# Kernel optimization log

Hardware: AMD Instinct MI355X
Metric: run time of the kernel (lower is better)

## Reference

```python
import jax, jax.numpy as jnp
import numpy as np

CAPS = 16          # num_capsules
DIM = 16           # capsule_dim
NUM_ROUTING = 3
L2_EPS = 1e-12     # tf.nn.l2_normalize epsilon


def setup_inputs() -> dict:
    key = jax.random.key(0)
    k1, k2 = jax.random.split(key)
    inputs = jax.random.normal(k1, (16, 64, 64, 128), dtype=jnp.float32)
    # Conv2D kernel, HWIO layout, fan-in scaled like glorot-ish init
    kernel = jax.random.normal(k2, (3, 3, 128, CAPS * DIM), dtype=jnp.float32) * 0.03
    bias = jnp.zeros((CAPS * DIM,), dtype=jnp.float32)
    return {"inputs": inputs, "kernel": kernel, "bias": bias}


def reference(inputs, kernel, bias):
    # Conv2D(caps*dim, 3x3, padding='same', activation='relu'), channels_last
    x = jax.lax.conv_general_dilated(
        inputs, kernel, window_strides=(1, 1), padding="SAME",
        dimension_numbers=("NHWC", "HWIO", "NHWC"))
    x = jax.nn.relu(x + bias)
    B, H, W, _ = x.shape
    x = x.reshape(B, H * W, CAPS, DIM)            # (B, N, C, D)
    b = jnp.zeros((B, H * W, CAPS), dtype=x.dtype)
    v = None
    for _ in range(NUM_ROUTING):
        c = jax.nn.softmax(b, axis=-1)             # over capsules
        s = jnp.einsum("bnc,bncd->bcd", c, x)      # weighted sum over spatial
        # tf.nn.l2_normalize along last axis
        v = s * jax.lax.rsqrt(jnp.maximum(jnp.sum(s * s, axis=-1, keepdims=True), L2_EPS))
        b = b + jnp.einsum("bncd,bcd->bnc", x, v)  # agreement update
    # tile v over spatial dims: (B,1,1,C*D) -> (B,H,W,C*D)
    out = jnp.broadcast_to(v.reshape(B, 1, 1, CAPS * DIM), (B, H, W, CAPS * DIM))
    return out
```

## Files before the change

kernel.cpp:

```cpp
#include <hip/hip_runtime.h>
#include <hip/hip_bf16.h>

typedef unsigned short u16;
typedef unsigned int   u32;

typedef __bf16 bf16x8 __attribute__((ext_vector_type(8)));
typedef float  f32x4  __attribute__((ext_vector_type(4)));

__device__ __forceinline__ u16 f2b(float f) {
    __hip_bfloat16 h = __float2bfloat16(f);
    u16 u; __builtin_memcpy(&u, &h, 2); return u;
}
__device__ __forceinline__ float blo(u32 u) { return __uint_as_float(u << 16); }
__device__ __forceinline__ float bhi(u32 u) { return __uint_as_float(u & 0xffff0000u); }

__global__ void k_prep(const float* __restrict__ wk,
                       u16* __restrict__ BF, float* __restrict__ stats) {
    int bx = blockIdx.x, tid = threadIdx.x;
    if (bx < 1152) {
        int t = bx * 256 + tid;
        int j  = t & 7;
        int n  = (t >> 3) & 255;
        int q  = (t >> 11) & 3;
        int kk = (t >> 13) & 3;
        int p  = t >> 15;
        BF[t] = f2b(wk[(p * 128 + kk * 32 + q * 8 + j) * 256 + n]);
    } else {
        stats[(bx - 1152) * 256 + tid] = 0.f;
    }
}

__launch_bounds__(256, 3)
__global__ void k_conv(const float* __restrict__ in, const u16* __restrict__ BF,
                       const float* __restrict__ bias,
                       u16* __restrict__ X, float* __restrict__ s0) {
    __shared__ u16 ldsA[12672];
    const int t = threadIdx.x;
    const int lane = t & 63, wid = t >> 6;
    const int q = lane >> 4, l15 = lane & 15;
    const int bb = blockIdx.x >> 6;
    const int h  = blockIdx.x & 63;
    const int wn0 = wid << 6;

#define STAGE(S) { \
    const int sb0 = wid * 396; \
    _Pragma("unroll") for (int i = 0; i < 7; ++i) { \
        int slot = sb0 + i * 64 + lane; \
        if (i < 6 || lane < 12) { \
            int pr = slot / 528; int rem = slot - pr * 528; \
            int wp = rem >> 3, cs = rem & 7; \
            int gc = (S) * 8 + (cs ^ (wp & 7)); \
            int y = h + pr - 1, x = wp - 1; \
            int inb = ((unsigned)y < 64u) & ((unsigned)x < 64u); \
            int ys = inb ? y : 0, xs = inb ? x : 0; \
            const float4* s4 = (const float4*)(in + \
                (((bb * 64 + ys) * 64 + xs) * 128 + gc * 8)); \
            float4 f0 = s4[0], f1 = s4[1]; \
            float zf = inb ? 1.f : 0.f; \
            u16 ov[8]; \
            ov[0]=f2b(f0.x*zf); ov[1]=f2b(f0.y*zf); ov[2]=f2b(f0.z*zf); ov[3]=f2b(f0.w*zf); \
            ov[4]=f2b(f1.x*zf); ov[5]=f2b(f1.y*zf); ov[6]=f2b(f1.z*zf); ov[7]=f2b(f1.w*zf); \
            uint4 wv; __builtin_memcpy(&wv, ov, 16); \
            *(uint4*)((char*)ldsA + slot * 16) = wv; \
        } \
    } }

#define LOADB4(B, P, S, KK) { \
    _Pragma("unroll") for (int ni = 0; ni < 4; ++ni) \
        B[ni] = *(const bf16x8*)(BFl + (P) * 32768 + \
                                 ((S) * 2 + (KK)) * 8192 + ni * 128); }

#define COMP4(B, DH, DW, KK) { \
    bf16x8 af[4]; \
    _Pragma("unroll") for (int mi = 0; mi < 4; ++mi) { \
        int wp = mi * 16 + l15 + (DW); \
        int swz = ((KK) * 4 + q) ^ (wp & 7); \
        af[mi] = *(const bf16x8*)((const char*)ldsA + \
            (((DH) * 528 + wp * 8 + swz) << 4)); \
    } \
    _Pragma("unroll") for (int mi = 0; mi < 4; ++mi) \
    _Pragma("unroll") for (int ni = 0; ni < 4; ++ni) \
        acc[mi][ni] = __builtin_amdgcn_mfma_f32_16x16x32_bf16( \
            af[mi], B[ni], acc[mi][ni], 0, 0, 0); }

#define HALF(S) { \
    LOADB4(B0, 0, S, 0); \
    LOADB4(B1, 0, S, 1); COMP4(B0, 0, 0, 0); \
    LOADB4(B0, 1, S, 0); COMP4(B1, 0, 0, 1); \
    LOADB4(B1, 1, S, 1); COMP4(B0, 0, 1, 0); \
    LOADB4(B0, 2, S, 0); COMP4(B1, 0, 1, 1); \
    LOADB4(B1, 2, S, 1); COMP4(B0, 0, 2, 0); \
    LOADB4(B0, 3, S, 0); COMP4(B1, 0, 2, 1); \
    LOADB4(B1, 3, S, 1); COMP4(B0, 1, 0, 0); \
    LOADB4(B0, 4, S, 0); COMP4(B1, 1, 0, 1); \
    LOADB4(B1, 4, S, 1); COMP4(B0, 1, 1, 0); \
    LOADB4(B0, 5, S, 0); COMP4(B1, 1, 1, 1); \
    LOADB4(B1, 5, S, 1); COMP4(B0, 1, 2, 0); \
    LOADB4(B0, 6, S, 0); COMP4(B1, 1, 2, 1); \
    LOADB4(B1, 6, S, 1); COMP4(B0, 2, 0, 0); \
    LOADB4(B0, 7, S, 0); COMP4(B1, 2, 0, 1); \
    LOADB4(B1, 7, S, 1); COMP4(B0, 2, 1, 0); \
    LOADB4(B0, 8, S, 0); COMP4(B1, 2, 1, 1); \
    LOADB4(B1, 8, S, 1); COMP4(B0, 2, 2, 0); \
                         COMP4(B1, 2, 2, 1); }

    const u16* BFl = BF + (q * 2048 + (wn0 + l15) * 8);

    f32x4 zero = {0.f, 0.f, 0.f, 0.f};
    f32x4 acc[4][4];
    #pragma unroll
    for (int mi = 0; mi < 4; ++mi)
        #pragma unroll
        for (int ni = 0; ni < 4; ++ni) acc[mi][ni] = zero;

    bf16x8 B0[4], B1[4];

    STAGE(0);
    __syncthreads();
    HALF(0);
    __syncthreads();

    STAGE(1);
    __syncthreads();
    HALF(1);

    float bv[4];
    #pragma unroll
    for (int ni = 0; ni < 4; ++ni) bv[ni] = bias[wn0 + ni * 16 + l15];
    float colsum[4] = {0.f, 0.f, 0.f, 0.f};
    u16* xrow = X + (((bb << 12) + (h << 6) + q * 4) * 256) + wn0 + l15;
    #pragma unroll
    for (int mi = 0; mi < 4; ++mi) {
        #pragma unroll
        for (int rr = 0; rr < 4; ++rr) {
            u16* xp = xrow + (mi * 16 + rr) * 256;
            #pragma unroll
            for (int ni = 0; ni < 4; ++ni) {
                float v = acc[mi][ni][rr] + bv[ni];
                v = v > 0.f ? v : 0.f;
                xp[ni * 16] = f2b(v);
                colsum[ni] += v;
            }
        }
    }
    #pragma unroll
    for (int ni = 0; ni < 4; ++ni) {
        float c = colsum[ni];
        c += __shfl_xor(c, 16);
        c += __shfl_xor(c, 32);
        if (lane < 16) atomicAdd(&s0[bb * 256 + wn0 + ni * 16 + l15], c);
    }
#undef STAGE
#undef LOADB4
#undef COMP4
#undef HALF
}

__launch_bounds__(256, 4)
__global__ void k_pass(const u16* __restrict__ X, const float* __restrict__ Sa,
                       const float* __restrict__ Sb, float* __restrict__ Sout,
                       int use2) {
    __shared__ float vs[272];
    __shared__ float red[4 * 272];
    const int t = threadIdx.x, b = blockIdx.y, chunk = blockIdx.x;
    const int c = t & 15, nl = t >> 4;
    const int lane = t & 63, wid = t >> 6;
    {
        float sa = Sa[b * 256 + t];
        float ss = sa * sa;
        #pragma unroll
        for (int off = 1; off < 16; off <<= 1) ss += __shfl_xor(ss, off);
        ss = ss < 1e-12f ? 1e-12f : ss;
        float vv = sa / sqrtf(ss);
        if (use2) {
            float sb = Sb[b * 256 + t];
            float s2v = sb * sb;
            #pragma unroll
            for (int off = 1; off < 16; off <<= 1) s2v += __shfl_xor(s2v, off);
            s2v = s2v < 1e-12f ? 1e-12f : s2v;
            vv += sb / sqrtf(s2v);
        }
        vs[(t >> 4) * 17 + (t & 15)] = vv;
    }
    const u16* xbase = X + ((b << 12) + chunk * 64 + nl) * 256 + c * 16;
    uint4 pa[8];
    #pragma unroll
    for (int r = 0; r < 4; ++r) {
        pa[2 * r]     = ((const uint4*)(xbase + r * 4096))[0];
        pa[2 * r + 1] = ((const uint4*)(xbase + r * 4096))[1];
    }
    __syncthreads();
    float vr[16];
    #pragma unroll
    for (int d = 0; d < 16; ++d) vr[d] = vs[c * 17 + d];

    float acc[16];
    #pragma unroll
    for (int d = 0; d < 16; ++d) acc[d] = 0.f;

    #pragma unroll
    for (int r = 0; r < 4; ++r) {
        u32 us[8];
        __builtin_memcpy(us, &pa[2 * r], 32);
        float xf[16];
        #pragma unroll
        for (int j = 0; j < 8; ++j) { xf[2*j] = blo(us[j]); xf[2*j+1] = bhi(us[j]); }
        float bvv = 0.f;
        #pragma unroll
        for (int d = 0; d < 16; ++d) bvv += xf[d] * vr[d];
        float e = __expf(bvv);
        float sm = e;
        #pragma unroll
        for (int off = 1; off < 16; off <<= 1) sm += __shfl_xor(sm, off);
        float w = e / sm;
        #pragma unroll
        for (int d = 0; d < 16; ++d) acc[d] += w * xf[d];
    }
    #pragma unroll
    for (int d = 0; d < 16; ++d) {
        acc[d] += __shfl_xor(acc[d], 16);
        acc[d] += __shfl_xor(acc[d], 32);
    }
    if (lane < 16) {
        #pragma unroll
        for (int d = 0; d < 16; ++d) red[wid * 272 + lane * 17 + d] = acc[d];
    }
    __syncthreads();
    {
        int c2 = t >> 4, d2 = t & 15;
        float tot = red[c2 * 17 + d2]       + red[272 + c2 * 17 + d2]
                  + red[544 + c2 * 17 + d2] + red[816 + c2 * 17 + d2];
        atomicAdd(&Sout[b * 256 + t], tot);
    }
}

__launch_bounds__(256, 4)
__global__ void k_bcast(const float* __restrict__ S, float* __restrict__ Out) {
    __shared__ float vls[256];
    int t = threadIdx.x, bx = blockIdx.x, b = blockIdx.y;
    float s = S[b * 256 + t];
    float ss = s * s;
    #pragma unroll
    for (int off = 1; off < 16; off <<= 1) ss += __shfl_xor(ss, off);
    ss = ss < 1e-12f ? 1e-12f : ss;
    vls[t] = s / sqrtf(ss);
    __syncthreads();
    float4 myv = ((const float4*)vls)[t & 63];
    float4* o = (float4*)Out + (long)b * 262144 + bx * 4096;
    #pragma unroll
    for (int j = 0; j < 16; ++j) o[j * 256 + t] = myv;
}

extern "C" void kernel_launch(void* const* d_in, const int* in_sizes, int n_in,
                              void* d_out, int out_size, void* d_ws, size_t ws_size,
                              hipStream_t stream) {
    const float* in   = (const float*)d_in[0];
    const float* wk   = (const float*)d_in[1];
    const float* bias = (const float*)d_in[2];
    float* out = (float*)d_out;
    char* ws = (char*)d_ws;

    const size_t OFF_BF  = 0;
    const size_t OFF_X   = 589824;
    const size_t OFF_ST  = 34144256;
    const size_t NEEDED  = OFF_ST + 3 * 16384;
    if (ws_size < NEEDED) return;

    u16* BF  = (u16*)(ws + OFF_BF);
    u16* X   = (u16*)(ws + OFF_X);
    float* s0 = (float*)(ws + OFF_ST);
    float* s2 = s0 + 4096;
    float* s3 = s2 + 4096;

    k_prep <<<1200, 256, 0, stream>>>(wk, BF, s0);
    k_conv <<<1024, 256, 0, stream>>>(in, BF, bias, X, s0);
    k_pass <<<dim3(64, 16), 256, 0, stream>>>(X, s0, s0, s2, 0);
    k_pass <<<dim3(64, 16), 256, 0, stream>>>(X, s0, s2, s3, 1);
    k_bcast<<<dim3(64, 16), 256, 0, stream>>>(s3, out);
}
```

Baseline: 181.9 us.

## Stage full input channel slab once with 512-thread blocks split over rows

The conv kernel now uses 512 threads (8 waves arranged 2x4) per output row. Each wave computes 32 pixels by 64 channels instead of 64 by 64. All 128 input channels are staged into LDS in a single pass, with every global load issued before the conversion and stores. This removes the second staging phase and two barriers and halves the accumulator registers per wave. The cost is twice the LDS per block and twice the B-fragment traffic per output, since each weight fragment now feeds only two M-tiles.

```diff
diff --git a/kernel.cpp b/kernel.cpp
--- a/kernel.cpp
+++ b/kernel.cpp
@@ -30,107 +30,129 @@
     }
 }
 
-__launch_bounds__(256, 3)
+__launch_bounds__(512, 4)
 __global__ void k_conv(const float* __restrict__ in, const u16* __restrict__ BF,
                        const float* __restrict__ bias,
                        u16* __restrict__ X, float* __restrict__ s0) {
-    __shared__ u16 ldsA[12672];
+    __shared__ u16 ldsA[25344];
     const int t = threadIdx.x;
     const int lane = t & 63, wid = t >> 6;
     const int q = lane >> 4, l15 = lane & 15;
+    const int wr = wid >> 2;
+    const int wc = wid & 3;
     const int bb = blockIdx.x >> 6;
     const int h  = blockIdx.x & 63;
-    const int wn0 = wid << 6;
-
-#define STAGE(S) { \
-    const int sb0 = wid * 396; \
+    const int wn0 = wc << 6;
+
+#define STAGE_ALL() { \
+    float4 fa[7], fb[7]; float zf[7]; \
     _Pragma("unroll") for (int i = 0; i < 7; ++i) { \
-        int slot = sb0 + i * 64 + lane; \
-        if (i < 6 || lane < 12) { \
-            int pr = slot / 528; int rem = slot - pr * 528; \
-            int wp = rem >> 3, cs = rem & 7; \
-            int gc = (S) * 8 + (cs ^ (wp & 7)); \
-            int y = h + pr - 1, x = wp - 1; \
-            int inb = ((unsigned)y < 64u) & ((unsigned)x < 64u); \
-            int ys = inb ? y : 0, xs = inb ? x : 0; \
-            const float4* s4 = (const float4*)(in + \
-                (((bb * 64 + ys) * 64 + xs) * 128 + gc * 8)); \
-            float4 f0 = s4[0], f1 = s4[1]; \
-            float zf = inb ? 1.f : 0.f; \
+        int slot = i * 512 + t; \
+        int ok = (i < 6) | (t < 96); \
+        int pr = slot / 1056; int rem = slot - pr * 1056; \
+        int wp = rem >> 4, cs = rem & 15; \
+        int gc = cs ^ (wp & 7); \
+        int y = h + pr - 1, x = wp - 1; \
+        int inb = ok & ((((unsigned)y < 64u) & ((unsigned)x < 64u)) ? 1 : 0); \
+        int ys = inb ? y : 0, xs = inb ? x : 0; \
+        const float4* s4 = (const float4*)(in + \
+            (((bb * 64 + ys) * 64 + xs) * 128 + gc * 8)); \
+        fa[i] = s4[0]; fb[i] = s4[1]; \
+        zf[i] = inb ? 1.f : 0.f; \
+    } \
+    _Pragma("unroll") for (int i = 0; i < 7; ++i) { \
+        if (i < 6 || t < 96) { \
+            int slot = i * 512 + t; \
             u16 ov[8]; \
-            ov[0]=f2b(f0.x*zf); ov[1]=f2b(f0.y*zf); ov[2]=f2b(f0.z*zf); ov[3]=f2b(f0.w*zf); \
-            ov[4]=f2b(f1.x*zf); ov[5]=f2b(f1.y*zf); ov[6]=f2b(f1.z*zf); ov[7]=f2b(f1.w*zf); \
+            ov[0]=f2b(fa[i].x*zf[i]); ov[1]=f2b(fa[i].y*zf[i]); \
+            ov[2]=f2b(fa[i].z*zf[i]); ov[3]=f2b(fa[i].w*zf[i]); \
+            ov[4]=f2b(fb[i].x*zf[i]); ov[5]=f2b(fb[i].y*zf[i]); \
+            ov[6]=f2b(fb[i].z*zf[i]); ov[7]=f2b(fb[i].w*zf[i]); \
             uint4 wv; __builtin_memcpy(&wv, ov, 16); \
             *(uint4*)((char*)ldsA + slot * 16) = wv; \
         } \
     } }
 
-#define LOADB4(B, P, S, KK) { \
+#define LOADB4(B, P, G) { \
     _Pragma("unroll") for (int ni = 0; ni < 4; ++ni) \
-        B[ni] = *(const bf16x8*)(BFl + (P) * 32768 + \
-                                 ((S) * 2 + (KK)) * 8192 + ni * 128); }
-
-#define COMP4(B, DH, DW, KK) { \
-    bf16x8 af[4]; \
-    _Pragma("unroll") for (int mi = 0; mi < 4; ++mi) { \
-        int wp = mi * 16 + l15 + (DW); \
-        int swz = ((KK) * 4 + q) ^ (wp & 7); \
+        B[ni] = *(const bf16x8*)(BFl + (P) * 32768 + (G) * 8192 + ni * 128); }
+
+#define COMP4(B, DH, DW, G) { \
+    bf16x8 af[2]; \
+    _Pragma("unroll") for (int mi = 0; mi < 2; ++mi) { \
+        int wp = wr * 32 + mi * 16 + l15 + (DW); \
+        int swz = ((G) * 4 + q) ^ (wp & 7); \
         af[mi] = *(const bf16x8*)((const char*)ldsA + \
-            (((DH) * 528 + wp * 8 + swz) << 4)); \
+            (((DH) * 1056 + wp * 16 + swz) << 4)); \
     } \
-    _Pragma("unroll") for (int mi = 0; mi < 4; ++mi) \
+    _Pragma("unroll") for (int mi = 0; mi < 2; ++mi) \
     _Pragma("unroll") for (int ni = 0; ni < 4; ++ni) \
         acc[mi][ni] = __builtin_amdgcn_mfma_f32_16x16x32_bf16( \
             af[mi], B[ni], acc[mi][ni], 0, 0, 0); }
 
-#define HALF(S) { \
-    LOADB4(B0, 0, S, 0); \
-    LOADB4(B1, 0, S, 1); COMP4(B0, 0, 0, 0); \
-    LOADB4(B0, 1, S, 0); COMP4(B1, 0, 0, 1); \
-    LOADB4(B1, 1, S, 1); COMP4(B0, 0, 1, 0); \
-    LOADB4(B0, 2, S, 0); COMP4(B1, 0, 1, 1); \
-    LOADB4(B1, 2, S, 1); COMP4(B0, 0, 2, 0); \
-    LOADB4(B0, 3, S, 0); COMP4(B1, 0, 2, 1); \
-    LOADB4(B1, 3, S, 1); COMP4(B0, 1, 0, 0); \
-    LOADB4(B0, 4, S, 0); COMP4(B1, 1, 0, 1); \
-    LOADB4(B1, 4, S, 1); COMP4(B0, 1, 1, 0); \
-    LOADB4(B0, 5, S, 0); COMP4(B1, 1, 1, 1); \
-    LOADB4(B1, 5, S, 1); COMP4(B0, 1, 2, 0); \
-    LOADB4(B0, 6, S, 0); COMP4(B1, 1, 2, 1); \
-    LOADB4(B1, 6, S, 1); COMP4(B0, 2, 0, 0); \
-    LOADB4(B0, 7, S, 0); COMP4(B1, 2, 0, 1); \
-    LOADB4(B1, 7, S, 1); COMP4(B0, 2, 1, 0); \
-    LOADB4(B0, 8, S, 0); COMP4(B1, 2, 1, 1); \
-    LOADB4(B1, 8, S, 1); COMP4(B0, 2, 2, 0); \
-                         COMP4(B1, 2, 2, 1); }
+#define CHAIN() { \
+    LOADB4(B0, 0, 2); COMP4(B1, 0, 0, 1); \
+    LOADB4(B1, 0, 3); COMP4(B0, 0, 0, 2); \
+    LOADB4(B0, 1, 0); COMP4(B1, 0, 0, 3); \
+    LOADB4(B1, 1, 1); COMP4(B0, 0, 1, 0); \
+    LOADB4(B0, 1, 2); COMP4(B1, 0, 1, 1); \
+    LOADB4(B1, 1, 3); COMP4(B0, 0, 1, 2); \
+    LOADB4(B0, 2, 0); COMP4(B1, 0, 1, 3); \
+    LOADB4(B1, 2, 1); COMP4(B0, 0, 2, 0); \
+    LOADB4(B0, 2, 2); COMP4(B1, 0, 2, 1); \
+    LOADB4(B1, 2, 3); COMP4(B0, 0, 2, 2); \
+    LOADB4(B0, 3, 0); COMP4(B1, 0, 2, 3); \
+    LOADB4(B1, 3, 1); COMP4(B0, 1, 0, 0); \
+    LOADB4(B0, 3, 2); COMP4(B1, 1, 0, 1); \
+    LOADB4(B1, 3, 3); COMP4(B0, 1, 0, 2); \
+    LOADB4(B0, 4, 0); COMP4(B1, 1, 0, 3); \
+    LOADB4(B1, 4, 1); COMP4(B0, 1, 1, 0); \
+    LOADB4(B0, 4, 2); COMP4(B1, 1, 1, 1); \
+    LOADB4(B1, 4, 3); COMP4(B0, 1, 1, 2); \
+    LOADB4(B0, 5, 0); COMP4(B1, 1, 1, 3); \
+    LOADB4(B1, 5, 1); COMP4(B0, 1, 2, 0); \
+    LOADB4(B0, 5, 2); COMP4(B1, 1, 2, 1); \
+    LOADB4(B1, 5, 3); COMP4(B0, 1, 2, 2); \
+    LOADB4(B0, 6, 0); COMP4(B1, 1, 2, 3); \
+    LOADB4(B1, 6, 1); COMP4(B0, 2, 0, 0); \
+    LOADB4(B0, 6, 2); COMP4(B1, 2, 0, 1); \
+    LOADB4(B1, 6, 3); COMP4(B0, 2, 0, 2); \
+    LOADB4(B0, 7, 0); COMP4(B1, 2, 0, 3); \
+    LOADB4(B1, 7, 1); COMP4(B0, 2, 1, 0); \
+    LOADB4(B0, 7, 2); COMP4(B1, 2, 1, 1); \
+    LOADB4(B1, 7, 3); COMP4(B0, 2, 1, 2); \
+    LOADB4(B0, 8, 0); COMP4(B1, 2, 1, 3); \
+    LOADB4(B1, 8, 1); COMP4(B0, 2, 2, 0); \
+    LOADB4(B0, 8, 2); COMP4(B1, 2, 2, 1); \
+    LOADB4(B1, 8, 3); COMP4(B0, 2, 2, 2); \
+                      COMP4(B1, 2, 2, 3); }
 
     const u16* BFl = BF + (q * 2048 + (wn0 + l15) * 8);
 
+    STAGE_ALL();
+
     f32x4 zero = {0.f, 0.f, 0.f, 0.f};
-    f32x4 acc[4][4];
-    #pragma unroll
-    for (int mi = 0; mi < 4; ++mi)
+    f32x4 acc[2][4];
+    #pragma unroll
+    for (int mi = 0; mi < 2; ++mi)
         #pragma unroll
         for (int ni = 0; ni < 4; ++ni) acc[mi][ni] = zero;
 
     bf16x8 B0[4], B1[4];
-
-    STAGE(0);
+    LOADB4(B0, 0, 0);
+    LOADB4(B1, 0, 1);
     __syncthreads();
-    HALF(0);
-    __syncthreads();
-
-    STAGE(1);
-    __syncthreads();
-    HALF(1);
+
+    COMP4(B0, 0, 0, 0);
+    CHAIN();
 
     float bv[4];
     #pragma unroll
     for (int ni = 0; ni < 4; ++ni) bv[ni] = bias[wn0 + ni * 16 + l15];
     float colsum[4] = {0.f, 0.f, 0.f, 0.f};
-    u16* xrow = X + (((bb << 12) + (h << 6) + q * 4) * 256) + wn0 + l15;
-    #pragma unroll
-    for (int mi = 0; mi < 4; ++mi) {
+    u16* xrow = X + (((bb << 12) + (h << 6) + wr * 32 + q * 4) * 256) + wn0 + l15;
+    #pragma unroll
+    for (int mi = 0; mi < 2; ++mi) {
         #pragma unroll
         for (int rr = 0; rr < 4; ++rr) {
             u16* xp = xrow + (mi * 16 + rr) * 256;
@@ -150,10 +172,10 @@
         c += __shfl_xor(c, 32);
         if (lane < 16) atomicAdd(&s0[bb * 256 + wn0 + ni * 16 + l15], c);
     }
-#undef STAGE
+#undef STAGE_ALL
 #undef LOADB4
 #undef COMP4
-#undef HALF
+#undef CHAIN
 }
 
 __launch_bounds__(256, 4)
@@ -273,7 +295,7 @@
     float* s3 = s2 + 4096;
 
     k_prep <<<1200, 256, 0, stream>>>(wk, BF, s0);
-    k_conv <<<1024, 256, 0, stream>>>(in, BF, bias, X, s0);
+    k_conv <<<1024, 512, 0, stream>>>(in, BF, bias, X, s0);
     k_pass <<<dim3(64, 16), 256, 0, stream>>>(X, s0, s0, s2, 0);
     k_pass <<<dim3(64, 16), 256, 0, stream>>>(X, s0, s2, s3, 1);
     k_bcast<<<dim3(64, 16), 256, 0, stream>>>(s3, out);
```

New measurement: 166.8 us. -8.3%, faster.
